# Kernel tuning notes

Measured on AMD Instinct MI355X. Metric: run time of the kernel, lower is better.

The kernel has to match this reference:

```python
import jax, jax.numpy as jnp
import numpy as np

N, E, D_IN, HID, HEADS, D_OUT = 50000, 500000, 128, 64, 8, 8
NEG_SLOPE = 0.2


def gat_conv(x, src, dst, W, a_src, a_dst, bias, concat):
    """PyG GATConv forward (with self-loops already appended to src/dst).
    x: [N, Fin], W: [Fin, H*C], a_src/a_dst: [H, C], bias: [H*C] or [C].
    """
    n = x.shape[0]
    H, C = a_src.shape
    h = (x @ W).reshape(n, H, C)                      # [N, H, C]
    alpha_src = jnp.sum(h * a_src, axis=-1)           # [N, H]
    alpha_dst = jnp.sum(h * a_dst, axis=-1)           # [N, H]
    e = alpha_src[src] + alpha_dst[dst]               # [E, H]
    e = jax.nn.leaky_relu(e, NEG_SLOPE)
    # segment softmax over destination node (every node has a self-loop)
    m = jax.ops.segment_max(e, dst, num_segments=n)   # [N, H]
    w = jnp.exp(e - m[dst])                           # [E, H]
    denom = jax.ops.segment_sum(w, dst, num_segments=n)
    alpha = w / (denom[dst] + 1e-16)                  # [E, H]
    msg = h[src] * alpha[..., None]                   # [E, H, C]
    out = jax.ops.segment_sum(msg, dst, num_segments=n)  # [N, H, C]
    out = out.reshape(n, H * C) if concat else out.mean(axis=1)
    return out + bias


def setup_inputs() -> dict:
    key = jax.random.key(0)
    ks = jax.random.split(key, 10)
    x = jax.random.normal(ks[0], (N, D_IN), dtype=jnp.float32)
    edge_index = jax.random.randint(ks[1], (2, E), 0, N, dtype=jnp.int32)
    s1 = 1.0 / np.sqrt(D_IN)
    s2 = 1.0 / np.sqrt(HID * HEADS)
    W1 = jax.random.normal(ks[2], (D_IN, HEADS * HID), dtype=jnp.float32) * s1
    a_src1 = jax.random.normal(ks[3], (HEADS, HID), dtype=jnp.float32) * 0.1
    a_dst1 = jax.random.normal(ks[4], (HEADS, HID), dtype=jnp.float32) * 0.1
    b1 = jnp.zeros((HEADS * HID,), dtype=jnp.float32)
    W2 = jax.random.normal(ks[5], (HEADS * HID, D_OUT), dtype=jnp.float32) * s2
    a_src2 = jax.random.normal(ks[6], (1, D_OUT), dtype=jnp.float32) * 0.1
    a_dst2 = jax.random.normal(ks[7], (1, D_OUT), dtype=jnp.float32) * 0.1
    b2 = jnp.zeros((D_OUT,), dtype=jnp.float32)
    return {"x": x, "edge_index": edge_index, "W1": W1, "a_src1": a_src1,
            "a_dst1": a_dst1, "b1": b1, "W2": W2, "a_src2": a_src2,
            "a_dst2": a_dst2, "b2": b2}


def reference(x, edge_index, W1, a_src1, a_dst1, b1, W2, a_src2, a_dst2, b2):
    n = x.shape[0]
    loops = jnp.arange(n, dtype=edge_index.dtype)
    src = jnp.concatenate([edge_index[0], loops])  # PyG adds self-loops
    dst = jnp.concatenate([edge_index[1], loops])
    h = jax.nn.relu(gat_conv(x, src, dst, W1, a_src1, a_dst1, b1, concat=True))
    out = gat_conv(h, src, dst, W2, a_src2, a_dst2, b2, concat=False)
    return out
```

## Files before the change

kernel.cpp:

```cpp
#include <hip/hip_runtime.h>
#include <stdint.h>

#define LEAKY(x) fmaxf((x), 0.2f * (x))

typedef short bf16x8 __attribute__((ext_vector_type(8)));
typedef float f32x4 __attribute__((ext_vector_type(4)));

__device__ inline float2 bf2_to_f2(uint32_t p) {
    return make_float2(__uint_as_float(p << 16), __uint_as_float(p & 0xffff0000u));
}
__device__ inline uint32_t pack_bf2(float x, float y) {
    uint32_t xb = __float_as_uint(x), yb = __float_as_uint(y);
    xb += 0x7fff + ((xb >> 16) & 1);
    yb += 0x7fff + ((yb >> 16) & 1);
    return (xb >> 16) | (yb & 0xffff0000u);
}
__device__ inline ushort to_bf16(float v) {
    uint32_t b = __float_as_uint(v);
    b += 0x7fff + ((b >> 16) & 1);
    return (ushort)(b >> 16);
}


__global__ __launch_bounds__(256) void degree_w1t_kernel(const int* __restrict__ dst,
                                                         int* __restrict__ deg, int E,
                                                         int nEb,
                                                         const float* __restrict__ W,
                                                         ushort* __restrict__ WT) {
    if ((int)blockIdx.x < nEb) {
        int e = blockIdx.x * 256 + threadIdx.x;
        if (e < E) atomicAdd(&deg[dst[e]], 1);
    } else {
        int bb = blockIdx.x - nEb;
        int c = bb * 64 + (threadIdx.x & 63);
        int k0 = (threadIdx.x >> 6) * 32;
        #pragma unroll
        for (int j = 0; j < 32; ++j)
            WT[(size_t)c * 128 + k0 + j] = to_bf16(W[(size_t)(k0 + j) * 512 + c]);
    }
}


__global__ __launch_bounds__(1024) void scan_fused_kernel(const int* __restrict__ deg,
                                                          int* __restrict__ off,
                                                          int* __restrict__ cur,
                                                          int* __restrict__ bflag,
                                                          int n, int nb) {
    __shared__ int wsum[16];
    __shared__ int sbase;
    int b = blockIdx.x, tid = threadIdx.x;
    int lane = tid & 63, wid = tid >> 6;
    int i0 = b * 4096 + tid * 4;
    int v0 = 0, v1 = 0, v2 = 0, v3 = 0;
    if (i0 + 3 < n) {
        int4 q = *(const int4*)(deg + i0);
        v0 = q.x; v1 = q.y; v2 = q.z; v3 = q.w;
    } else {
        if (i0 + 0 < n) v0 = deg[i0];
        if (i0 + 1 < n) v1 = deg[i0 + 1];
        if (i0 + 2 < n) v2 = deg[i0 + 2];
        if (i0 + 3 < n) v3 = deg[i0 + 3];
    }
    int s = v0 + v1 + v2 + v3;
    int x = s;
    #pragma unroll
    for (int d2 = 1; d2 < 64; d2 <<= 1) {
        int y = __shfl_up(x, d2);
        if (lane >= d2) x += y;
    }
    if (lane == 63) wsum[wid] = x;
    __syncthreads();
    if (tid < 16) {
        int t = wsum[tid];
        #pragma unroll
        for (int d2 = 1; d2 < 16; d2 <<= 1) {
            int y = __shfl_up(t, d2, 16);
            if (tid >= d2) t += y;
        }
        wsum[tid] = t;
    }
    __syncthreads();
    int wbase = wid ? wsum[wid - 1] : 0;
    int total = wsum[15];
    if (tid == 0) {
        atomicExch(&bflag[b], total + 1);
        int base = 0;
        for (int i = 0; i < b; ++i) {
            int v;
            while ((v = atomicAdd(&bflag[i], 0)) == 0) {}
            base += v - 1;
        }
        sbase = base;
    }
    __syncthreads();
    int base = sbase;
    int pre = base + wbase + (x - s);
    if (i0 + 3 < n) {
        int4 q = make_int4(pre, pre + v0, pre + v0 + v1, pre + v0 + v1 + v2);
        *(int4*)(off + i0) = q;
        *(int4*)(cur + i0) = q;
    } else {
        int p0 = pre, p1 = pre + v0, p2 = pre + v0 + v1, p3 = pre + v0 + v1 + v2;
        if (i0 + 0 < n) { off[i0] = p0; cur[i0] = p0; }
        if (i0 + 1 < n) { off[i0 + 1] = p1; cur[i0 + 1] = p1; }
        if (i0 + 2 < n) { off[i0 + 2] = p2; cur[i0 + 2] = p2; }
        if (i0 + 3 < n) { off[i0 + 3] = p3; cur[i0 + 3] = p3; }
    }
    if (b == nb - 1 && tid == 0) off[n] = base + total;
}


__global__ __launch_bounds__(256) void gemm1_scatter_kernel(
        const float* __restrict__ x, const ushort* __restrict__ W1T,
        const float* __restrict__ a_src, const float* __restrict__ a_dst,
        uint32_t* __restrict__ h1, float* __restrict__ asrc1,
        float* __restrict__ adst1, int N, int nGb,
        const int* __restrict__ esrc, const int* __restrict__ edst,
        int* __restrict__ cur, int* __restrict__ csr_src, int E) {
    __shared__ __align__(16) ushort As[128][128];
    __shared__ __align__(16) ushort Bs[128][128];
    int tid = threadIdx.x;
    if ((int)blockIdx.x >= nGb) {
        int e = (blockIdx.x - nGb) * 256 + tid;
        if (e < E) {
            int d = edst[e];
            int p = atomicAdd(&cur[d], 1);
            csr_src[p] = esrc[e];
        }
        return;
    }
    int row0 = blockIdx.x * 128;

    {
        int g = tid & 15;
        int r4 = tid >> 4;
        #pragma unroll
        for (int pass = 0; pass < 8; ++pass) {
            int r = r4 + pass * 16;
            int gr = row0 + r;
            float4 v0 = make_float4(0.f, 0.f, 0.f, 0.f), v1 = v0;
            if (gr < N) {
                v0 = *(const float4*)(x + (size_t)gr * 128 + g * 8);
                v1 = *(const float4*)(x + (size_t)gr * 128 + g * 8 + 4);
            }
            uint4 pk = make_uint4(pack_bf2(v0.x, v0.y), pack_bf2(v0.z, v0.w),
                                  pack_bf2(v1.x, v1.y), pack_bf2(v1.z, v1.w));
            *(uint4*)&As[r][(g ^ (r & 7)) * 8] = pk;
        }
    }
    __syncthreads();

    int wave = tid >> 6, lane = tid & 63;
    int wr = wave >> 1, wc = wave & 1;
    int lg = lane >> 4, lr = lane & 15;

    for (int cb = 0; cb < 4; ++cb) {
        int c0 = cb * 128;
        {
            int g = tid & 15;
            int r4 = tid >> 4;
            #pragma unroll
            for (int pass = 0; pass < 8; ++pass) {
                int r = r4 + pass * 16;
                uint4 q = *(const uint4*)(W1T + (size_t)(c0 + r) * 128 + g * 8);
                *(uint4*)&Bs[r][(g ^ (r & 7)) * 8] = q;
            }
        }
        __syncthreads();

        f32x4 acc[4][4] = {};
        #pragma unroll
        for (int kk = 0; kk < 4; ++kk) {
            bf16x8 a[4], b[4];
            int gk = kk * 4 + lg;
            #pragma unroll
            for (int mi = 0; mi < 4; ++mi) {
                int r = wr * 64 + mi * 16 + lr;
                a[mi] = *(const bf16x8*)&As[r][(gk ^ (r & 7)) * 8];
            }
            #pragma unroll
            for (int nj = 0; nj < 4; ++nj) {
                int r = wc * 64 + nj * 16 + lr;
                b[nj] = *(const bf16x8*)&Bs[r][(gk ^ (r & 7)) * 8];
            }
            #pragma unroll
            for (int mi = 0; mi < 4; ++mi)
                #pragma unroll
                for (int nj = 0; nj < 4; ++nj)
                    acc[mi][nj] = __builtin_amdgcn_mfma_f32_16x16x32_bf16(
                        a[mi], b[nj], acc[mi][nj], 0, 0, 0);
        }

        int hh = cb * 2 + wc;
        float as4[4], ad4[4];
        #pragma unroll
        for (int nj = 0; nj < 4; ++nj) {
            as4[nj] = a_src[hh * 64 + nj * 16 + lr];
            ad4[nj] = a_dst[hh * 64 + nj * 16 + lr];
        }
        #pragma unroll
        for (int mi = 0; mi < 4; ++mi) {
            #pragma unroll
            for (int reg = 0; reg < 4; ++reg) {
                int row = row0 + wr * 64 + mi * 16 + lg * 4 + reg;
                float v0 = acc[mi][0][reg], v1 = acc[mi][1][reg];
                float v2 = acc[mi][2][reg], v3 = acc[mi][3][reg];
                float ps = v0 * as4[0] + v1 * as4[1] + v2 * as4[2] + v3 * as4[3];
                float pd = v0 * ad4[0] + v1 * ad4[1] + v2 * ad4[2] + v3 * ad4[3];
                #pragma unroll
                for (int m = 1; m < 16; m <<= 1) {
                    ps += __shfl_xor(ps, m);
                    pd += __shfl_xor(pd, m);
                }
                bool store_row = (row < N);
                if (store_row && lr == 0) {
                    asrc1[(size_t)row * 8 + hh] = ps;
                    adst1[(size_t)row * 8 + hh] = pd;
                }
                float p0 = __shfl_xor(v0, 1), p1 = __shfl_xor(v1, 1);
                float p2 = __shfl_xor(v2, 1), p3 = __shfl_xor(v3, 1);
                if (store_row && (lr & 1) == 0) {
                    size_t base = (size_t)row * 256 + ((c0 + wc * 64 + lr) >> 1);
                    h1[base + 0]  = pack_bf2(v0, p0);
                    h1[base + 8]  = pack_bf2(v1, p1);
                    h1[base + 16] = pack_bf2(v2, p2);
                    h1[base + 24] = pack_bf2(v3, p3);
                }
            }
        }
        __syncthreads();
    }
}


__global__ __launch_bounds__(256) void agg1_fused_kernel(
        const uint4* __restrict__ h1, const float* __restrict__ asrc,
        const float* __restrict__ adst, const int* __restrict__ off,
        const int* __restrict__ csr_src, const float* __restrict__ b1,
        const float* __restrict__ W2, const float* __restrict__ a_src2,
        const float* __restrict__ a_dst2, float* __restrict__ h2,
        float* __restrict__ as2, float* __restrict__ ad2, int N) {
    __shared__ __align__(16) float w2s[64 * 68];
    int tid = threadIdx.x;
    #pragma unroll
    for (int q = 0; q < 4; ++q) {
        float4 v = ((const float4*)W2)[tid * 4 + q];
        int g = tid * 16 + q * 4;
        *(float4*)&w2s[(g >> 6) * 68 + (g & 63)] = v;
    }
    __syncthreads();

    int n = (blockIdx.x * blockDim.x + tid) >> 6;
    int lane = tid & 63;
    if (n >= N) return;
    int hd = lane >> 3;
    float ad = adst[(size_t)n * 8 + hd];
    float2 acc2[4];
    float d;
    {
        float w = __expf(LEAKY(asrc[(size_t)n * 8 + hd] + ad));
        d = w;
        uint4 p = h1[(size_t)n * 64 + lane];
        float2 c0 = bf2_to_f2(p.x), c1 = bf2_to_f2(p.y);
        float2 c2 = bf2_to_f2(p.z), c3 = bf2_to_f2(p.w);
        acc2[0] = make_float2(w * c0.x, w * c0.y);
        acc2[1] = make_float2(w * c1.x, w * c1.y);
        acc2[2] = make_float2(w * c2.x, w * c2.y);
        acc2[3] = make_float2(w * c3.x, w * c3.y);
    }
    auto addp = [&](uint4 p, float w) {
        float2 c0 = bf2_to_f2(p.x), c1 = bf2_to_f2(p.y);
        float2 c2 = bf2_to_f2(p.z), c3 = bf2_to_f2(p.w);
        d += w;
        acc2[0].x += w * c0.x; acc2[0].y += w * c0.y;
        acc2[1].x += w * c1.x; acc2[1].y += w * c1.y;
        acc2[2].x += w * c2.x; acc2[2].y += w * c2.y;
        acc2[3].x += w * c3.x; acc2[3].y += w * c3.y;
    };
    int t = off[n], tend = off[n + 1];
    for (; t + 3 < tend; t += 4) {
        int s0 = csr_src[t], s1 = csr_src[t + 1];
        int s2 = csr_src[t + 2], s3 = csr_src[t + 3];
        uint4 p0 = h1[(size_t)s0 * 64 + lane];
        uint4 p1 = h1[(size_t)s1 * 64 + lane];
        uint4 p2 = h1[(size_t)s2 * 64 + lane];
        uint4 p3 = h1[(size_t)s3 * 64 + lane];
        float w0 = __expf(LEAKY(asrc[(size_t)s0 * 8 + hd] + ad));
        float w1 = __expf(LEAKY(asrc[(size_t)s1 * 8 + hd] + ad));
        float w2 = __expf(LEAKY(asrc[(size_t)s2 * 8 + hd] + ad));
        float w3 = __expf(LEAKY(asrc[(size_t)s3 * 8 + hd] + ad));
        addp(p0, w0); addp(p1, w1); addp(p2, w2); addp(p3, w3);
    }
    for (; t < tend; ++t) {
        int s = csr_src[t];
        uint4 p = h1[(size_t)s * 64 + lane];
        float w = __expf(LEAKY(asrc[(size_t)s * 8 + hd] + ad));
        addp(p, w);
    }
    float inv = 1.f / (d + 1e-16f);
    float4 b0 = *(const float4*)(b1 + lane * 8);
    float4 b4 = *(const float4*)(b1 + lane * 8 + 4);
    float o[8];
    o[0] = fmaxf(acc2[0].x * inv + b0.x, 0.f);
    o[1] = fmaxf(acc2[0].y * inv + b0.y, 0.f);
    o[2] = fmaxf(acc2[1].x * inv + b0.z, 0.f);
    o[3] = fmaxf(acc2[1].y * inv + b0.w, 0.f);
    o[4] = fmaxf(acc2[2].x * inv + b4.x, 0.f);
    o[5] = fmaxf(acc2[2].y * inv + b4.y, 0.f);
    o[6] = fmaxf(acc2[3].x * inv + b4.z, 0.f);
    o[7] = fmaxf(acc2[3].y * inv + b4.w, 0.f);
    asm volatile("" ::: "memory");
    const float* wrow = &w2s[lane * 68];
    float pc[8] = {};
    #pragma unroll
    for (int j = 0; j < 8; ++j) {
        float4 wa = *(const float4*)(wrow + j * 8);
        float4 wb = *(const float4*)(wrow + j * 8 + 4);
        float ov = o[j];
        pc[0] += ov * wa.x; pc[1] += ov * wa.y;
        pc[2] += ov * wa.z; pc[3] += ov * wa.w;
        pc[4] += ov * wb.x; pc[5] += ov * wb.y;
        pc[6] += ov * wb.z; pc[7] += ov * wb.w;
    }
    #pragma unroll
    for (int m = 1; m < 64; m <<= 1)
        #pragma unroll
        for (int c = 0; c < 8; ++c)
            pc[c] += __shfl_xor(pc[c], m);
    if (lane < 8) {
        float myv = 0.f;
        #pragma unroll
        for (int c = 0; c < 8; ++c) if (lane == c) myv = pc[c];
        h2[(size_t)n * 8 + lane] = myv;
        if (lane == 0) {
            float pa = 0.f, pb = 0.f;
            #pragma unroll
            for (int c = 0; c < 8; ++c) { pa += pc[c] * a_src2[c]; pb += pc[c] * a_dst2[c]; }
            as2[n] = pa;
            ad2[n] = pb;
        }
    }
}


__global__ __launch_bounds__(256) void agg2_kernel(const float* __restrict__ h2,
                                                   const float* __restrict__ as2,
                                                   const float* __restrict__ ad2,
                                                   const int* __restrict__ off,
                                                   const int* __restrict__ csr_src,
                                                   const float* __restrict__ b2,
                                                   float* __restrict__ out, int N) {
    int gid = blockIdx.x * blockDim.x + threadIdx.x;
    int n = gid >> 3, c = gid & 7;
    if (n >= N) return;
    float adn = ad2[n];
    float w = __expf(LEAKY(as2[n] + adn));
    float d = w;
    float acc = w * h2[(size_t)n * 8 + c];
    int t = off[n], tend = off[n + 1];
    for (; t + 1 < tend; t += 2) {
        int s0 = csr_src[t], s1 = csr_src[t + 1];
        float h0 = h2[(size_t)s0 * 8 + c];
        float h1v = h2[(size_t)s1 * 8 + c];
        float w0 = __expf(LEAKY(as2[s0] + adn));
        float w1 = __expf(LEAKY(as2[s1] + adn));
        d += w0 + w1;
        acc += w0 * h0 + w1 * h1v;
    }
    if (t < tend) {
        int s = csr_src[t];
        float ws = __expf(LEAKY(as2[s] + adn));
        d += ws;
        acc += ws * h2[(size_t)s * 8 + c];
    }
    out[(size_t)n * 8 + c] = acc / (d + 1e-16f) + b2[c];
}


extern "C" void kernel_launch(void* const* d_in, const int* in_sizes, int n_in,
                              void* d_out, int out_size, void* d_ws, size_t ws_size,
                              hipStream_t stream) {
    const float* x      = (const float*)d_in[0];
    const int*   ei     = (const int*)d_in[1];
    const float* W1     = (const float*)d_in[2];
    const float* a_src1 = (const float*)d_in[3];
    const float* a_dst1 = (const float*)d_in[4];
    const float* b1     = (const float*)d_in[5];
    const float* W2     = (const float*)d_in[6];
    const float* a_src2 = (const float*)d_in[7];
    const float* a_dst2 = (const float*)d_in[8];
    const float* b2     = (const float*)d_in[9];

    int N = in_sizes[0] / 128;
    int E = in_sizes[1] / 2;
    const int* src = ei;
    const int* dst = ei + E;

    char* w = (char*)d_ws;
    size_t o = 0;
    auto alloc = [&](size_t bytes) {
        void* p = w + o;
        o = (o + bytes + 255) & ~(size_t)255;
        return p;
    };
    uint32_t* h1     = (uint32_t*)alloc((size_t)N * 256 * 4);
    float*    asrc1  = (float*)alloc((size_t)N * 8 * 4);
    float*    adst1  = (float*)alloc((size_t)N * 8 * 4);
    float*    h2     = (float*)alloc((size_t)N * 8 * 4);
    float*    as2    = (float*)alloc((size_t)N * 4);
    float*    ad2    = (float*)alloc((size_t)N * 4);
    int*      deg    = (int*)alloc((size_t)N * 4);
    int*      bflag  = (int*)alloc(64 * 4);
    int*      offb   = (int*)alloc((size_t)(N + 1) * 4);
    int*      cur    = (int*)alloc((size_t)N * 4);
    int*      csrs   = (int*)alloc((size_t)E * 4);
    ushort*   W1T    = (ushort*)alloc((size_t)512 * 128 * 2);

    size_t zero_bytes = ((size_t)N * 4 + 255 & ~(size_t)255) + 64 * 4;
    hipMemsetAsync(deg, 0, zero_bytes, stream);

    int nb = (N + 4095) / 4096;
    int nEb = (E + 255) / 256;
    int nGb = (N + 127) / 128;
    degree_w1t_kernel<<<nEb + 8, 256, 0, stream>>>(dst, deg, E, nEb, W1, W1T);
    scan_fused_kernel<<<nb, 1024, 0, stream>>>(deg, offb, cur, bflag, N, nb);

    gemm1_scatter_kernel<<<nGb + nEb, 256, 0, stream>>>(
        x, W1T, a_src1, a_dst1, h1, asrc1, adst1, N, nGb,
        src, dst, cur, csrs, E);

    agg1_fused_kernel<<<((size_t)N * 64 + 255) / 256, 256, 0, stream>>>(
        (const uint4*)h1, asrc1, adst1, offb, csrs, b1, W2, a_src2, a_dst2,
        h2, as2, ad2, N);

    agg2_kernel<<<((size_t)N * 8 + 255) / 256, 256, 0, stream>>>(h2, as2, ad2, offb, csrs, b2,
                                                                 (float*)d_out, N);
}
```

Baseline: 169.4 us.

## Fold attention vectors into W1 and pre-convert x to bf16 in pre-kernel

```diff
diff --git a/kernel.cpp b/kernel.cpp
--- a/kernel.cpp
+++ b/kernel.cpp
@@ -22,21 +22,51 @@
 }
 
 
-__global__ __launch_bounds__(256) void degree_w1t_kernel(const int* __restrict__ dst,
-                                                         int* __restrict__ deg, int E,
-                                                         int nEb,
-                                                         const float* __restrict__ W,
-                                                         ushort* __restrict__ WT) {
-    if ((int)blockIdx.x < nEb) {
-        int e = blockIdx.x * 256 + threadIdx.x;
+__global__ __launch_bounds__(256) void pre_kernel(const int* __restrict__ dst,
+                                                  int* __restrict__ deg, int E, int nEb,
+                                                  const float* __restrict__ W,
+                                                  ushort* __restrict__ WT,
+                                                  const float* __restrict__ x,
+                                                  ushort* __restrict__ xb, size_t nx,
+                                                  const float* __restrict__ a_src,
+                                                  const float* __restrict__ a_dst,
+                                                  ushort* __restrict__ va, int nXb) {
+    int b = blockIdx.x;
+    if (b < nEb) {
+        int e = b * 256 + threadIdx.x;
         if (e < E) atomicAdd(&deg[dst[e]], 1);
-    } else {
-        int bb = blockIdx.x - nEb;
+    } else if (b < nEb + 8) {
+        int bb = b - nEb;
         int c = bb * 64 + (threadIdx.x & 63);
         int k0 = (threadIdx.x >> 6) * 32;
         #pragma unroll
         for (int j = 0; j < 32; ++j)
             WT[(size_t)c * 128 + k0 + j] = to_bf16(W[(size_t)(k0 + j) * 512 + c]);
+    } else if (b < nEb + 8 + nXb) {
+        size_t i0 = (size_t)(b - nEb - 8) * 2048 + (size_t)threadIdx.x * 8;
+        if (i0 < nx) {
+            float4 v0 = *(const float4*)(x + i0);
+            float4 v1 = *(const float4*)(x + i0 + 4);
+            uint4 pk = make_uint4(pack_bf2(v0.x, v0.y), pack_bf2(v0.z, v0.w),
+                                  pack_bf2(v1.x, v1.y), pack_bf2(v1.z, v1.w));
+            *(uint4*)(xb + i0) = pk;
+        }
+    } else {
+        int k = threadIdx.x;
+        if (k < 128) {
+            #pragma unroll
+            for (int h = 0; h < 8; ++h) {
+                float s = 0.f, d = 0.f;
+                #pragma unroll 8
+                for (int c = 0; c < 64; ++c) {
+                    float wv = W[(size_t)k * 512 + h * 64 + c];
+                    s += wv * a_src[h * 64 + c];
+                    d += wv * a_dst[h * 64 + c];
+                }
+                va[(size_t)h * 128 + k] = to_bf16(s);
+                va[(size_t)(8 + h) * 128 + k] = to_bf16(d);
+            }
+        }
     }
 }
 
@@ -111,14 +141,15 @@
 
 
 __global__ __launch_bounds__(256) void gemm1_scatter_kernel(
-        const float* __restrict__ x, const ushort* __restrict__ W1T,
-        const float* __restrict__ a_src, const float* __restrict__ a_dst,
+        const ushort* __restrict__ xb, const ushort* __restrict__ W1T,
+        const ushort* __restrict__ va,
         uint32_t* __restrict__ h1, float* __restrict__ asrc1,
         float* __restrict__ adst1, int N, int nGb,
         const int* __restrict__ esrc, const int* __restrict__ edst,
         int* __restrict__ cur, int* __restrict__ csr_src, int E) {
     __shared__ __align__(16) ushort As[128][128];
     __shared__ __align__(16) ushort Bs[128][128];
+    __shared__ __align__(16) ushort Vs[16][128];
     int tid = threadIdx.x;
     if ((int)blockIdx.x >= nGb) {
         int e = (blockIdx.x - nGb) * 256 + tid;
@@ -130,23 +161,18 @@
         return;
     }
     int row0 = blockIdx.x * 128;
+    int g = tid & 15, r4 = tid >> 4;
 
     {
-        int g = tid & 15;
-        int r4 = tid >> 4;
         #pragma unroll
         for (int pass = 0; pass < 8; ++pass) {
             int r = r4 + pass * 16;
             int gr = row0 + r;
-            float4 v0 = make_float4(0.f, 0.f, 0.f, 0.f), v1 = v0;
-            if (gr < N) {
-                v0 = *(const float4*)(x + (size_t)gr * 128 + g * 8);
-                v1 = *(const float4*)(x + (size_t)gr * 128 + g * 8 + 4);
-            }
-            uint4 pk = make_uint4(pack_bf2(v0.x, v0.y), pack_bf2(v0.z, v0.w),
-                                  pack_bf2(v1.x, v1.y), pack_bf2(v1.z, v1.w));
-            *(uint4*)&As[r][(g ^ (r & 7)) * 8] = pk;
-        }
+            uint4 q = *(const uint4*)(xb + (size_t)gr * 128 + (size_t)((g ^ (r & 7)) * 8));
+            *(uint4*)&As[r][g * 8] = q;
+        }
+        uint4 qv = *(const uint4*)(va + (size_t)r4 * 128 + (size_t)((g ^ (r4 & 7)) * 8));
+        *(uint4*)&Vs[r4][g * 8] = qv;
     }
     __syncthreads();
 
@@ -154,11 +180,35 @@
     int wr = wave >> 1, wc = wave & 1;
     int lg = lane >> 4, lr = lane & 15;
 
+    if (wc == 0) {
+        f32x4 av[4] = {};
+        #pragma unroll
+        for (int kk = 0; kk < 4; ++kk) {
+            int gk = kk * 4 + lg;
+            bf16x8 bv = *(const bf16x8*)&Vs[lr][(gk ^ (lr & 7)) * 8];
+            #pragma unroll
+            for (int mi = 0; mi < 4; ++mi) {
+                int r = wr * 64 + mi * 16 + lr;
+                bf16x8 am = *(const bf16x8*)&As[r][(gk ^ (r & 7)) * 8];
+                av[mi] = __builtin_amdgcn_mfma_f32_16x16x32_bf16(am, bv, av[mi], 0, 0, 0);
+            }
+        }
+        #pragma unroll
+        for (int mi = 0; mi < 4; ++mi)
+            #pragma unroll
+            for (int reg = 0; reg < 4; ++reg) {
+                int row = row0 + wr * 64 + mi * 16 + lg * 4 + reg;
+                if (row < N) {
+                    float v = av[mi][reg];
+                    if (lr < 8) asrc1[(size_t)row * 8 + lr] = v;
+                    else        adst1[(size_t)row * 8 + (lr - 8)] = v;
+                }
+            }
+    }
+
     for (int cb = 0; cb < 4; ++cb) {
         int c0 = cb * 128;
         {
-            int g = tid & 15;
-            int r4 = tid >> 4;
             #pragma unroll
             for (int pass = 0; pass < 8; ++pass) {
                 int r = r4 + pass * 16;
@@ -191,13 +241,6 @@
                         a[mi], b[nj], acc[mi][nj], 0, 0, 0);
         }
 
-        int hh = cb * 2 + wc;
-        float as4[4], ad4[4];
-        #pragma unroll
-        for (int nj = 0; nj < 4; ++nj) {
-            as4[nj] = a_src[hh * 64 + nj * 16 + lr];
-            ad4[nj] = a_dst[hh * 64 + nj * 16 + lr];
-        }
         #pragma unroll
         for (int mi = 0; mi < 4; ++mi) {
             #pragma unroll
@@ -205,21 +248,9 @@
                 int row = row0 + wr * 64 + mi * 16 + lg * 4 + reg;
                 float v0 = acc[mi][0][reg], v1 = acc[mi][1][reg];
                 float v2 = acc[mi][2][reg], v3 = acc[mi][3][reg];
-                float ps = v0 * as4[0] + v1 * as4[1] + v2 * as4[2] + v3 * as4[3];
-                float pd = v0 * ad4[0] + v1 * ad4[1] + v2 * ad4[2] + v3 * ad4[3];
-                #pragma unroll
-                for (int m = 1; m < 16; m <<= 1) {
-                    ps += __shfl_xor(ps, m);
-                    pd += __shfl_xor(pd, m);
-                }
-                bool store_row = (row < N);
-                if (store_row && lr == 0) {
-                    asrc1[(size_t)row * 8 + hh] = ps;
-                    adst1[(size_t)row * 8 + hh] = pd;
-                }
                 float p0 = __shfl_xor(v0, 1), p1 = __shfl_xor(v1, 1);
                 float p2 = __shfl_xor(v2, 1), p3 = __shfl_xor(v3, 1);
-                if (store_row && (lr & 1) == 0) {
+                if (row < N && (lr & 1) == 0) {
                     size_t base = (size_t)row * 256 + ((c0 + wc * 64 + lr) >> 1);
                     h1[base + 0]  = pack_bf2(v0, p0);
                     h1[base + 8]  = pack_bf2(v1, p1);
@@ -404,6 +435,7 @@
         return p;
     };
     uint32_t* h1     = (uint32_t*)alloc((size_t)N * 256 * 4);
+    ushort*   xb     = (ushort*)alloc((size_t)(N + 128) * 128 * 2);
     float*    asrc1  = (float*)alloc((size_t)N * 8 * 4);
     float*    adst1  = (float*)alloc((size_t)N * 8 * 4);
     float*    h2     = (float*)alloc((size_t)N * 8 * 4);
@@ -415,18 +447,22 @@
     int*      cur    = (int*)alloc((size_t)N * 4);
     int*      csrs   = (int*)alloc((size_t)E * 4);
     ushort*   W1T    = (ushort*)alloc((size_t)512 * 128 * 2);
+    ushort*   va     = (ushort*)alloc((size_t)16 * 128 * 2);
 
     size_t zero_bytes = ((size_t)N * 4 + 255 & ~(size_t)255) + 64 * 4;
     hipMemsetAsync(deg, 0, zero_bytes, stream);
 
+    size_t nx = (size_t)N * 128;
     int nb = (N + 4095) / 4096;
     int nEb = (E + 255) / 256;
     int nGb = (N + 127) / 128;
-    degree_w1t_kernel<<<nEb + 8, 256, 0, stream>>>(dst, deg, E, nEb, W1, W1T);
+    int nXb = (int)((nx + 2047) / 2048);
+    pre_kernel<<<nEb + 8 + nXb + 1, 256, 0, stream>>>(dst, deg, E, nEb, W1, W1T,
+                                                      x, xb, nx, a_src1, a_dst1, va, nXb);
     scan_fused_kernel<<<nb, 1024, 0, stream>>>(deg, offb, cur, bflag, N, nb);
 
     gemm1_scatter_kernel<<<nGb + nEb, 256, 0, stream>>>(
-        x, W1T, a_src1, a_dst1, h1, asrc1, adst1, N, nGb,
+        xb, W1T, va, h1, asrc1, adst1, N, nGb,
         src, dst, cur, csrs, E);
 
     agg1_fused_kernel<<<((size_t)N * 64 + 255) / 256, 256, 0, stream>>>(
```

After: 201.8 us. +19.1%, slower.
